# Performance work log

Hardware: AMD Instinct MI355X
Metric: run time of the kernel (lower is better)

The kernel has to match this reference:

```python
import jax, jax.numpy as jnp
import numpy as np
from jax.ops import segment_sum

N_NODES = 50000
N_EDGES = 400000
D_IN = 128
HIDDEN = [128, 128]
D_OUT = 64
ALPHA = 0.5


def _glorot(key, shape):
    fan_in, fan_out = shape
    lim = jnp.sqrt(6.0 / (fan_in + fan_out))
    return jax.random.uniform(key, shape, jnp.float32, -lim, lim)


def setup_inputs() -> dict:
    key = jax.random.key(0)
    ks = jax.random.split(key, 16)
    x = jax.random.normal(ks[0], (N_NODES, D_IN), jnp.float32)
    edge_index = jax.random.randint(ks[1], (2, N_EDGES), 0, N_NODES, jnp.int64)
    theta = jax.random.uniform(ks[2], (N_EDGES,), jnp.float32)
    return {
        "x": x,
        "edge_index": edge_index,
        "theta": theta,
        "W1_s2d": _glorot(ks[3], (D_IN, HIDDEN[0])),
        "W1_d2s": _glorot(ks[4], (D_IN, HIDDEN[0])),
        "b1_s2d": jnp.zeros((HIDDEN[0],), jnp.float32),
        "b1_d2s": jnp.zeros((HIDDEN[0],), jnp.float32),
        "W2_s2d": _glorot(ks[5], (HIDDEN[0], HIDDEN[1])),
        "W2_d2s": _glorot(ks[6], (HIDDEN[0], HIDDEN[1])),
        "b2_s2d": jnp.zeros((HIDDEN[1],), jnp.float32),
        "b2_d2s": jnp.zeros((HIDDEN[1],), jnp.float32),
        "W_ro": _glorot(ks[7], (HIDDEN[1], D_OUT)),
        "b_ro": jnp.zeros((D_OUT,), jnp.float32),
    }


def _fuzzy_laplacian(edge_index, theta, num_nodes):
    # bidirectional duplication + self loops (self_loop=True, edge_weight=1)
    senders, receivers = edge_index[0], edge_index[1]
    loop = jnp.arange(num_nodes, dtype=senders.dtype)
    cs = jnp.concatenate((senders, receivers, loop))
    cr = jnp.concatenate((receivers, senders, loop))
    c2, s2 = jnp.cos(theta) ** 2, jnp.sin(theta) ** 2
    ones = jnp.ones((num_nodes,), theta.dtype)
    # real(e^{i t})^2 = cos^2 t ; exp(i(pi/2 - t)) -> real^2 = sin^2 t
    out_w = jnp.concatenate((c2, s2, ones))
    in_w = jnp.concatenate((s2, c2, ones))
    deg_s = segment_sum(out_w, cs, num_segments=num_nodes) + 1e-12
    deg_r = segment_sum(in_w, cs, num_segments=num_nodes) + 1e-12
    dis_s = jnp.where(deg_s > 1e11, 0.0, jax.lax.rsqrt(deg_s))
    dis_r = jnp.where(deg_r > 1e11, 0.0, jax.lax.rsqrt(deg_r))
    w_s2d = dis_s[cs] * out_w * dis_r[cr]
    w_d2s = dis_r[cs] * in_w * dis_s[cr]
    return cs, cr, w_s2d, w_d2s


def _forward(x, edge_index, theta, W1_s2d, W1_d2s, b1_s2d, b1_d2s,
             W2_s2d, W2_d2s, b2_s2d, b2_d2s, W_ro, b_ro):
    num_nodes = x.shape[0]
    cs, cr, w_s2d, w_d2s = _fuzzy_laplacian(edge_index, theta, num_nodes)
    layers = [(W1_s2d, W1_d2s, b1_s2d, b1_d2s), (W2_s2d, W2_d2s, b2_s2d, b2_d2s)]
    for Ws, Wd, bs, bd in layers:
        xs = x[cs]  # [2E+N, F] gather
        agg_s = segment_sum(xs * w_s2d[:, None], cr, num_segments=num_nodes)
        agg_d = segment_sum(xs * w_d2s[:, None], cr, num_segments=num_nodes)
        x = ALPHA * (agg_s @ Ws + bs) + (1.0 - ALPHA) * (agg_d @ Wd + bd)
        x = jax.nn.relu(x)
    return x @ W_ro + b_ro


def reference(x, edge_index, theta, W1_s2d, W1_d2s, b1_s2d, b1_d2s,
              W2_s2d, W2_d2s, b2_s2d, b2_d2s, W_ro, b_ro):
    return _forward(x, edge_index, theta, W1_s2d, W1_d2s, b1_s2d, b1_d2s,
                    W2_s2d, W2_d2s, b2_s2d, b2_d2s, W_ro, b_ro)
```

## Files before the change

### kernel.cpp

```cpp
#include <hip/hip_runtime.h>
#include <hip/hip_fp16.h>

#define N_NODES 50000
#define N_EDGES 400000
#define CSR_E (2 * N_EDGES + N_NODES)
#define NCH 10
#define CHW 5000
#define NE2 (N_NODES * NCH)
#define EB 1563
#define PB 288

typedef unsigned short ushort_t;
typedef unsigned int uint_t;
typedef __attribute__((ext_vector_type(8))) short bf16x8;
typedef __attribute__((ext_vector_type(4))) float f32x4;

__device__ __forceinline__ float bf2f(ushort_t u) {
    return __uint_as_float(((uint_t)u) << 16);
}
__device__ __forceinline__ ushort_t f2bf(float f) {
    uint_t b = __float_as_uint(f);
    b += 0x7FFFu + ((b >> 16) & 1u);
    return (ushort_t)(b >> 16);
}
__device__ __forceinline__ uint_t packw(float a, float b) {
    return ((uint_t)__half_as_ushort(__float2half(b)) << 16) |
           (uint_t)__half_as_ushort(__float2half(a));
}
__device__ __forceinline__ float unpl(uint_t w) {
    return __half2float(__ushort_as_half((ushort_t)(w & 0xffffu)));
}
__device__ __forceinline__ float unph(uint_t w) {
    return __half2float(__ushort_as_half((ushort_t)(w >> 16)));
}


__device__ int g_est;
__device__ int g_is16;
__device__ __align__(8) float2 g_dis2[N_NODES];
__device__ int g_cnt2[NE2];
__device__ int g_offs2[NE2 + 1];
__device__ uint_t g_rank[N_EDGES];
__device__ uint_t g_scanst[512];
__device__ __align__(16) uint4 g_estage[N_EDGES];
__device__ __align__(16) uint2 g_csr8[CSR_E];
__device__ __align__(16) ushort_t g_h1[(size_t)N_NODES * 128];
__device__ __align__(16) ushort_t g_xcvt[(size_t)N_NODES * 128];
__device__ __align__(16) ushort_t g_bp1[8 * 128 * 32];
__device__ __align__(16) ushort_t g_bp2[8 * 128 * 32];
__device__ __align__(16) ushort_t g_bp3[4 * 64 * 32];
__device__ float g_bc1[128];
__device__ float g_bc2[128];
__device__ float g_bro[64];


__global__ __launch_bounds__(256) void init_all(const uint_t* __restrict__ xw,
                                                const int* __restrict__ eidx,
                                                const float* __restrict__ x32) {
    __shared__ int s_flags;
    if (threadIdx.x < 64) {
        uint_t w = xw[threadIdx.x];
        int elo = (w >> 7) & 0xFF;
        unsigned long long mb = __ballot(elo >= 100 && elo <= 150);
        unsigned long long me = __ballot(eidx[2 * threadIdx.x + 1] != 0);
        if (threadIdx.x == 0) {
            int is16 = (__popcll(mb) >= 48) ? 1 : 0;
            int est = me ? 1 : 2;
            s_flags = is16 | (est << 1);
        }
    }
    __syncthreads();
    int is16 = s_flags & 1;
    int t = blockIdx.x * 256 + threadIdx.x;
    if (t == 0) {
        g_is16 = is16;
        g_est = s_flags >> 1;
    }
    if (t < 512) g_scanst[t] = 0;
    if (t < N_NODES) {
        int sc = t / CHW;
#pragma unroll
        for (int c = 0; c < NCH; c++) g_cnt2[t * NCH + c] = (c == sc) ? 1 : 0;
    }
    if (!is16 && t < N_NODES * 128 / 8) {
        const float4* p = (const float4*)(x32 + t * 8);
        float4 a = p[0], b = p[1];
        ushort4 o0, o1;
        o0.x = f2bf(a.x); o0.y = f2bf(a.y); o0.z = f2bf(a.z); o0.w = f2bf(a.w);
        o1.x = f2bf(b.x); o1.y = f2bf(b.y); o1.z = f2bf(b.z); o1.w = f2bf(b.w);
        *(ushort4*)(g_xcvt + t * 8) = o0;
        *(ushort4*)(g_xcvt + t * 8 + 4) = o1;
    }
}


__global__ __launch_bounds__(256) void edge_prep(
    const int* __restrict__ eidx, const ushort_t* __restrict__ th16, const float* __restrict__ th32,
    const ushort_t* W1s16, const float* W1s32, const ushort_t* W1d16, const float* W1d32,
    const ushort_t* b1s16, const float* b1s32, const ushort_t* b1d16, const float* b1d32,
    const ushort_t* W2s16, const float* W2s32, const ushort_t* W2d16, const float* W2d32,
    const ushort_t* b2s16, const float* b2s32, const ushort_t* b2d16, const float* b2d32,
    const ushort_t* Wro16, const float* Wro32, const ushort_t* bro16, const float* bro32) {
    int gb = blockIdx.x;
    if (gb < EB) {
        int e = gb * 256 + threadIdx.x;
        if (e >= N_EDGES) return;
        int st = g_est;
        int s = eidx[(size_t)e * st];
        int r = eidx[((size_t)N_EDGES + e) * st];
        float t = g_is16 ? bf2f(th16[e]) : th32[e];
        float sn, cs_;
        sincosf(t, &sn, &cs_);
        float c2 = cs_ * cs_;
        float s2 = sn * sn;
        g_estage[e] = make_uint4((uint_t)s, (uint_t)r, __float_as_uint(c2), __float_as_uint(s2));
        int rf = atomicAdd(&g_cnt2[r * NCH + s / CHW], 1);
        int rr = atomicAdd(&g_cnt2[s * NCH + r / CHW], 1);
        g_rank[e] = (uint_t)rf | ((uint_t)rr << 16);
        return;
    }
    int is16 = g_is16;
    int t = (gb - EB) * 256 + threadIdx.x;
    if (t < 2 * 32768) {
        int layer = t >> 15;
        int i = t & 32767;
        const ushort_t* Ws16 = layer ? W2s16 : W1s16;
        const float* Ws32 = layer ? W2s32 : W1s32;
        const ushort_t* Wd16 = layer ? W2d16 : W1d16;
        const float* Wd32 = layer ? W2d32 : W1d32;
        ushort_t* Bp = layer ? g_bp2 : g_bp1;
        int k = i >> 7, n = i & 127;
        ushort_t v;
        if (k < 128) {
            int idx = k * 128 + n;
            v = is16 ? Ws16[idx] : f2bf(Ws32[idx]);
        } else {
            int idx = (k - 128) * 128 + n;
            v = is16 ? Wd16[idx] : f2bf(Wd32[idx]);
        }
        int kb = k >> 5, kk = k & 31;
        Bp[((kb * 128 + n) << 5) + kk] = v;
        if (i < 128) {
            const ushort_t* bs16 = layer ? b2s16 : b1s16;
            const float* bs32 = layer ? b2s32 : b1s32;
            const ushort_t* bd16 = layer ? b2d16 : b1d16;
            const float* bd32 = layer ? b2d32 : b1d32;
            float a = is16 ? bf2f(bs16[i]) : bs32[i];
            float b = is16 ? bf2f(bd16[i]) : bd32[i];
            (layer ? g_bc2 : g_bc1)[i] = 0.5f * (a + b);
        }
    } else {
        int i = t - 2 * 32768;
        int k = i >> 6, n = i & 63;
        ushort_t v = is16 ? Wro16[i] : f2bf(Wro32[i]);
        int kb = k >> 5, kk = k & 31;
        g_bp3[((kb * 64 + n) << 5) + kk] = v;
        if (i < 64) g_bro[i] = is16 ? bf2f(bro16[i]) : bro32[i];
    }
}


__global__ __launch_bounds__(1024) void scan_lb() {
    __shared__ int sd[1024];
    __shared__ int s_ex;
    int b = blockIdx.x;
    int t = threadIdx.x;
    int i = b * 1024 + t;
    int v = (i < NE2) ? g_cnt2[i] : 0;
    sd[t] = v;
    __syncthreads();
    for (int o = 1; o < 1024; o <<= 1) {
        int tv = (t >= o) ? sd[t - o] : 0;
        __syncthreads();
        sd[t] += tv;
        __syncthreads();
    }
    int incl = sd[t];
    int agg = sd[1023];
    if (t == 0) {
        atomicExch(&g_scanst[b], ((b == 0 ? 2u : 1u) << 20) | (uint_t)agg);
    }
    if (t < 64) {
        int ex = 0;
        if (b > 0) {
            int j = b - 1;
            while (true) {
                int idx = j - 63 + t;
                uint_t wv = (idx >= 0) ? atomicAdd(&g_scanst[idx], 0u) : (2u << 20);
                uint_t fl = wv >> 20;
                unsigned long long m2 = __ballot(fl == 2u);
                unsigned long long m0 = __ballot(fl == 0u);
                if (m2 != 0ull) {
                    int p = 63 - __clzll(m2);
                    unsigned long long above = (p == 63) ? 0ull : (~0ull << (p + 1));
                    if ((m0 & above) != 0ull) continue;
                    int contrib = (t >= p) ? (int)(wv & 0xFFFFFu) : 0;
#pragma unroll
                    for (int o = 1; o < 64; o <<= 1) contrib += __shfl_xor(contrib, o);
                    ex += contrib;
                    break;
                } else {
                    if (m0 != 0ull) continue;
                    int contrib = (int)(wv & 0xFFFFFu);
#pragma unroll
                    for (int o = 1; o < 64; o <<= 1) contrib += __shfl_xor(contrib, o);
                    ex += contrib;
                    j -= 64;
                }
            }
        }
        if (t == 0) {
            atomicExch(&g_scanst[b], (2u << 20) | (uint_t)(ex + agg));
            s_ex = ex;
        }
    }
    __syncthreads();
    if (i < NE2) g_offs2[i] = incl - v + s_ex;
    if (b == 0 && t == 0) g_offs2[NE2] = CSR_E;
}


__global__ __launch_bounds__(256) void fill_all() {
    int e = blockIdx.x * 256 + threadIdx.x;
    if (e < N_EDGES) {
        uint4 stg = g_estage[e];
        int s = (int)stg.x;
        int r = (int)stg.y;
        float c2 = __uint_as_float(stg.z);
        float s2 = __uint_as_float(stg.w);
        uint_t rk = g_rank[e];
        int pf = g_offs2[r * NCH + s / CHW] + (int)(rk & 0xffffu);
        int pr = g_offs2[s * NCH + r / CHW] + (int)(rk >> 16);
        g_csr8[pf] = make_uint2((uint_t)s, packw(c2, s2));
        g_csr8[pr] = make_uint2((uint_t)r, packw(s2, c2));
    }
    if (e < N_NODES) {
        g_csr8[g_offs2[e * NCH + e / CHW]] = make_uint2((uint_t)e, packw(1.0f, 1.0f));
    }
}


__global__ __launch_bounds__(256) void deg_pass() {
    int n = blockIdx.x * 256 + threadIdx.x;
    if (n >= N_NODES) return;
    int kb = g_offs2[n * NCH];
    int ke = g_offs2[n * NCH + NCH];
    float ds = 0.f, dr = 0.f;
    for (int k = kb; k < ke; k++) {
        uint_t w = g_csr8[k].y;
        ds += unph(w);
        dr += unpl(w);
    }
    g_dis2[n] = make_float2(rsqrtf(ds + 1e-12f), rsqrtf(dr + 1e-12f));
}


template <int LAYER>
__global__ __launch_bounds__(256) void fused_layer(const ushort_t* __restrict__ xext,
                                                   void* __restrict__ outp) {
    __shared__ ushort_t tA[16 * 256];
    __shared__ ushort_t tH[(LAYER == 1) ? 16 * 128 : 1];
    int w = threadIdx.x >> 6;
    int lane = threadIdx.x & 63;
    int gsel = lane >> 4;
    int r = lane & 15;
    int lrow = w * 4 + gsel;
    int node = blockIdx.x * 16 + lrow;
    const ushort_t* xin = (LAYER == 0) ? (g_is16 ? xext : g_xcvt) : g_h1;

    int ks = g_offs2[node * NCH];
    int ke = g_offs2[node * NCH + NCH];
    int c0 = ke - ks;
    int cmax = c0;
    cmax = max(cmax, __shfl_xor(cmax, 16));
    cmax = max(cmax, __shfl_xor(cmax, 32));

    float accS[8], accD[8];
#pragma unroll
    for (int f = 0; f < 8; f++) { accS[f] = 0.f; accD[f] = 0.f; }

    uint2 ecur = g_csr8[ks + min(r, c0 - 1)];
    int lbase = lane & 48;
    for (int k = 0; k < cmax; k += 16) {
        uint2 enext = ecur;
        if (k + 16 < cmax) enext = g_csr8[ks + min(k + 16 + r, c0 - 1)];
#pragma unroll
        for (int h = 0; h < 4; h++) {
            int kh = k + h * 4;
            if (kh >= cmax) break;
            uint_t eys[4];
            float2 ds2[4];
            bf16x8 vs[4];
#pragma unroll
            for (int j = 0; j < 4; j++) {
                int jj = h * 4 + j;
                uint_t ex = (uint_t)__shfl((int)ecur.x, lbase | jj, 64);
                eys[j] = (uint_t)__shfl((int)ecur.y, lbase | jj, 64);
                ds2[j] = g_dis2[ex];
                vs[j] = *(const bf16x8*)(xin + (size_t)ex * 128 + r * 8);
            }
#pragma unroll
            for (int j = 0; j < 4; j++) {
                bool val = (kh + j) < c0;
                float ws_ = val ? ds2[j].x * unpl(eys[j]) : 0.f;
                float wd_ = val ? ds2[j].y * unph(eys[j]) : 0.f;
#pragma unroll
                for (int f = 0; f < 8; f++) {
                    float xv = bf2f((ushort_t)vs[j][f]);
                    accS[f] = fmaf(ws_, xv, accS[f]);
                    accD[f] = fmaf(wd_, xv, accD[f]);
                }
            }
        }
        ecur = enext;
    }

    float2 dn = g_dis2[node];
    float fs = 0.5f * dn.y;
    float fd = 0.5f * dn.x;
    uint_t oS[4], oD[4];
#pragma unroll
    for (int p = 0; p < 4; p++) {
        oS[p] = ((uint_t)f2bf(accS[2 * p + 1] * fs) << 16) | (uint_t)f2bf(accS[2 * p] * fs);
        oD[p] = ((uint_t)f2bf(accD[2 * p + 1] * fd) << 16) | (uint_t)f2bf(accD[2 * p] * fd);
    }
    int swA = (lrow & 7) << 4;
    *(uint4*)((char*)tA + ((lrow * 512 + r * 16) ^ swA)) = make_uint4(oS[0], oS[1], oS[2], oS[3]);
    *(uint4*)((char*)tA + ((lrow * 512 + 256 + r * 16) ^ swA)) = make_uint4(oD[0], oD[1], oD[2], oD[3]);
    __syncthreads();

    int cc = lane & 15;
    int q = lane >> 4;
    int csw = (cc & 7) << 4;
    const ushort_t* Bp = (LAYER == 0) ? g_bp1 : g_bp2;
    const float* bias = (LAYER == 0) ? g_bc1 : g_bc2;
    f32x4 acc0 = {0.f, 0.f, 0.f, 0.f};
    f32x4 acc1 = {0.f, 0.f, 0.f, 0.f};
#pragma unroll
    for (int kb = 0; kb < 8; kb++) {
        bf16x8 a = *(const bf16x8*)((const char*)tA + ((cc * 512 + kb * 64 + q * 16) ^ csw));
        bf16x8 b0 = *(const bf16x8*)(Bp + (((kb * 128 + w * 32 + cc) << 5) + q * 8));
        bf16x8 b1 = *(const bf16x8*)(Bp + (((kb * 128 + w * 32 + 16 + cc) << 5) + q * 8));
        acc0 = __builtin_amdgcn_mfma_f32_16x16x32_bf16(a, b0, acc0, 0, 0, 0);
        acc1 = __builtin_amdgcn_mfma_f32_16x16x32_bf16(a, b1, acc1, 0, 0, 0);
    }
    int mb = blockIdx.x * 16;
    float bi0 = bias[w * 32 + cc];
    float bi1 = bias[w * 32 + 16 + cc];
    if (LAYER == 0) {
#pragma unroll
        for (int rr = 0; rr < 4; rr++) {
            int m = mb + q * 4 + rr;
            g_h1[(size_t)m * 128 + w * 32 + cc] = f2bf(fmaxf(acc0[rr] + bi0, 0.f));
            g_h1[(size_t)m * 128 + w * 32 + 16 + cc] = f2bf(fmaxf(acc1[rr] + bi1, 0.f));
        }
    } else {
#pragma unroll
        for (int rr = 0; rr < 4; rr++) {
            int ml = q * 4 + rr;
            int msw = (ml & 7) << 4;
            *(ushort_t*)((char*)tH + ((ml * 256 + (w * 32 + cc) * 2) ^ msw)) =
                f2bf(fmaxf(acc0[rr] + bi0, 0.f));
            *(ushort_t*)((char*)tH + ((ml * 256 + (w * 32 + 16 + cc) * 2) ^ msw)) =
                f2bf(fmaxf(acc1[rr] + bi1, 0.f));
        }
        __syncthreads();
        f32x4 a3 = {0.f, 0.f, 0.f, 0.f};
#pragma unroll
        for (int kb = 0; kb < 4; kb++) {
            bf16x8 a = *(const bf16x8*)((const char*)tH + ((cc * 256 + kb * 64 + q * 16) ^ csw));
            bf16x8 b = *(const bf16x8*)(g_bp3 + (((kb * 64 + w * 16 + cc) << 5) + q * 8));
            a3 = __builtin_amdgcn_mfma_f32_16x16x32_bf16(a, b, a3, 0, 0, 0);
        }
        int is16 = g_is16;
        float bi = g_bro[w * 16 + cc];
#pragma unroll
        for (int rr = 0; rr < 4; rr++) {
            int m = mb + q * 4 + rr;
            float v = a3[rr] + bi;
            if (is16)
                ((ushort_t*)outp)[(size_t)m * 64 + w * 16 + cc] = f2bf(v);
            else
                ((float*)outp)[(size_t)m * 64 + w * 16 + cc] = v;
        }
    }
}


static inline int cdiv(int a, int b) { return (a + b - 1) / b; }

extern "C" void kernel_launch(void* const* d_in, const int* in_sizes, int n_in,
                              void* d_out, int out_size, void* d_ws, size_t ws_size,
                              hipStream_t stream) {
    const void* x = d_in[0];
    const int* eidx = (const int*)d_in[1];
    const void* theta = d_in[2];
    const void* W1s = d_in[3];
    const void* W1d = d_in[4];
    const void* b1s = d_in[5];
    const void* b1d = d_in[6];
    const void* W2s = d_in[7];
    const void* W2d = d_in[8];
    const void* b2s = d_in[9];
    const void* b2d = d_in[10];
    const void* Wro = d_in[11];
    const void* bro = d_in[12];
    (void)in_sizes; (void)n_in; (void)out_size; (void)d_ws; (void)ws_size;

    const int NB2 = cdiv(NE2, 1024);

    init_all<<<cdiv(N_NODES * 128 / 8, 256), 256, 0, stream>>>(
        (const uint_t*)x, eidx, (const float*)x);
    edge_prep<<<EB + PB, 256, 0, stream>>>(
        eidx, (const ushort_t*)theta, (const float*)theta,
        (const ushort_t*)W1s, (const float*)W1s, (const ushort_t*)W1d, (const float*)W1d,
        (const ushort_t*)b1s, (const float*)b1s, (const ushort_t*)b1d, (const float*)b1d,
        (const ushort_t*)W2s, (const float*)W2s, (const ushort_t*)W2d, (const float*)W2d,
        (const ushort_t*)b2s, (const float*)b2s, (const ushort_t*)b2d, (const float*)b2d,
        (const ushort_t*)Wro, (const float*)Wro, (const ushort_t*)bro, (const float*)bro);
    scan_lb<<<NB2, 1024, 0, stream>>>();
    fill_all<<<cdiv(N_EDGES, 256), 256, 0, stream>>>();
    deg_pass<<<cdiv(N_NODES, 256), 256, 0, stream>>>();

    const int AB = N_NODES / 16;
    fused_layer<0><<<AB, 256, 0, stream>>>((const ushort_t*)x, nullptr);
    fused_layer<1><<<AB, 256, 0, stream>>>(nullptr, d_out);
}
```

Measured before the change: 263.1 us.

## Fold init into edge_prep, pre-scale CSR weights, pack rank into staging

Merges the init kernel into edge_prep. The x fp32-to-bf16 conversion runs as extra grid-strided blocks, and the count/scan-state reset moves into scan_lb and fill_all so state is reset for the next call. It drops the separate rank buffer by storing it in the staging record's fourth word and recomputes sin² as 1-cos². A new finalize_w pass multiplies the source-node normalisation into the packed fp16 edge weights, so both fused layers no longer gather g_dis2 per edge. The cost is one extra pass over the CSR array, plus fp16 rounding of the pre-multiplied weights.

Measured after the change: 260.0 us. No clear change (-1.2%).

```diff
diff --git a/kernel.cpp b/kernel.cpp
--- a/kernel.cpp
+++ b/kernel.cpp
@@ -9,6 +9,7 @@
 #define NE2 (N_NODES * NCH)
 #define EB 1563
 #define PB 288
+#define CB 1024
 
 typedef unsigned short ushort_t;
 typedef unsigned int uint_t;
@@ -40,7 +41,6 @@
 __device__ __align__(8) float2 g_dis2[N_NODES];
 __device__ int g_cnt2[NE2];
 __device__ int g_offs2[NE2 + 1];
-__device__ uint_t g_rank[N_EDGES];
 __device__ uint_t g_scanst[512];
 __device__ __align__(16) uint4 g_estage[N_EDGES];
 __device__ __align__(16) uint2 g_csr8[CSR_E];
@@ -54,9 +54,14 @@
 __device__ float g_bro[64];
 
 
-__global__ __launch_bounds__(256) void init_all(const uint_t* __restrict__ xw,
-                                                const int* __restrict__ eidx,
-                                                const float* __restrict__ x32) {
+__global__ __launch_bounds__(256) void edge_prep(
+    const uint_t* __restrict__ xw,
+    const int* __restrict__ eidx, const ushort_t* __restrict__ th16, const float* __restrict__ th32,
+    const ushort_t* W1s16, const float* W1s32, const ushort_t* W1d16, const float* W1d32,
+    const ushort_t* b1s16, const float* b1s32, const ushort_t* b1d16, const float* b1d32,
+    const ushort_t* W2s16, const float* W2s32, const ushort_t* W2d16, const float* W2d32,
+    const ushort_t* b2s16, const float* b2s32, const ushort_t* b2d16, const float* b2d32,
+    const ushort_t* Wro16, const float* Wro32, const ushort_t* bro16, const float* bro32) {
     __shared__ int s_flags;
     if (threadIdx.x < 64) {
         uint_t w = xw[threadIdx.x];
@@ -64,98 +69,85 @@
         unsigned long long mb = __ballot(elo >= 100 && elo <= 150);
         unsigned long long me = __ballot(eidx[2 * threadIdx.x + 1] != 0);
         if (threadIdx.x == 0) {
-            int is16 = (__popcll(mb) >= 48) ? 1 : 0;
-            int est = me ? 1 : 2;
-            s_flags = is16 | (est << 1);
+            int is16v = (__popcll(mb) >= 48) ? 1 : 0;
+            int estv = me ? 1 : 2;
+            s_flags = is16v | (estv << 1);
         }
     }
     __syncthreads();
     int is16 = s_flags & 1;
-    int t = blockIdx.x * 256 + threadIdx.x;
-    if (t == 0) {
+    int est = s_flags >> 1;
+    int gb = blockIdx.x;
+    if (gb == 0 && threadIdx.x == 0) {
         g_is16 = is16;
-        g_est = s_flags >> 1;
-    }
-    if (t < 512) g_scanst[t] = 0;
-    if (t < N_NODES) {
-        int sc = t / CHW;
-#pragma unroll
-        for (int c = 0; c < NCH; c++) g_cnt2[t * NCH + c] = (c == sc) ? 1 : 0;
-    }
-    if (!is16 && t < N_NODES * 128 / 8) {
-        const float4* p = (const float4*)(x32 + t * 8);
+        g_est = est;
+    }
+    if (gb < EB) {
+        int e = gb * 256 + threadIdx.x;
+        if (e >= N_EDGES) return;
+        int s = eidx[(size_t)e * est];
+        int r = eidx[((size_t)N_EDGES + e) * est];
+        float t = is16 ? bf2f(th16[e]) : th32[e];
+        float sn, cs_;
+        sincosf(t, &sn, &cs_);
+        float c2 = cs_ * cs_;
+        int rf = atomicAdd(&g_cnt2[r * NCH + s / CHW], 1);
+        int rr = atomicAdd(&g_cnt2[s * NCH + r / CHW], 1);
+        g_estage[e] = make_uint4((uint_t)s, (uint_t)r, __float_as_uint(c2),
+                                 (uint_t)rf | ((uint_t)rr << 16));
+        return;
+    }
+    if (gb < EB + PB) {
+        int t = (gb - EB) * 256 + threadIdx.x;
+        if (t < 2 * 32768) {
+            int layer = t >> 15;
+            int i = t & 32767;
+            const ushort_t* Ws16 = layer ? W2s16 : W1s16;
+            const float* Ws32 = layer ? W2s32 : W1s32;
+            const ushort_t* Wd16 = layer ? W2d16 : W1d16;
+            const float* Wd32 = layer ? W2d32 : W1d32;
+            ushort_t* Bp = layer ? g_bp2 : g_bp1;
+            int k = i >> 7, n = i & 127;
+            ushort_t v;
+            if (k < 128) {
+                int idx = k * 128 + n;
+                v = is16 ? Ws16[idx] : f2bf(Ws32[idx]);
+            } else {
+                int idx = (k - 128) * 128 + n;
+                v = is16 ? Wd16[idx] : f2bf(Wd32[idx]);
+            }
+            int kb = k >> 5, kk = k & 31;
+            Bp[((kb * 128 + n) << 5) + kk] = v;
+            if (i < 128) {
+                const ushort_t* bs16 = layer ? b2s16 : b1s16;
+                const float* bs32 = layer ? b2s32 : b1s32;
+                const ushort_t* bd16 = layer ? b2d16 : b1d16;
+                const float* bd32 = layer ? b2d32 : b1d32;
+                float a = is16 ? bf2f(bs16[i]) : bs32[i];
+                float b = is16 ? bf2f(bd16[i]) : bd32[i];
+                (layer ? g_bc2 : g_bc1)[i] = 0.5f * (a + b);
+            }
+        } else {
+            int i = t - 2 * 32768;
+            int k = i >> 6, n = i & 63;
+            ushort_t v = is16 ? Wro16[i] : f2bf(Wro32[i]);
+            int kb = k >> 5, kk = k & 31;
+            g_bp3[((kb * 64 + n) << 5) + kk] = v;
+            if (i < 64) g_bro[i] = is16 ? bf2f(bro16[i]) : bro32[i];
+        }
+        return;
+    }
+    if (is16) return;
+    const float* x32 = (const float*)xw;
+    const int total = N_NODES * 128 / 8;
+    for (int i = (gb - EB - PB) * 256 + threadIdx.x; i < total; i += CB * 256) {
+        const float4* p = (const float4*)(x32 + (size_t)i * 8);
         float4 a = p[0], b = p[1];
         ushort4 o0, o1;
         o0.x = f2bf(a.x); o0.y = f2bf(a.y); o0.z = f2bf(a.z); o0.w = f2bf(a.w);
         o1.x = f2bf(b.x); o1.y = f2bf(b.y); o1.z = f2bf(b.z); o1.w = f2bf(b.w);
-        *(ushort4*)(g_xcvt + t * 8) = o0;
-        *(ushort4*)(g_xcvt + t * 8 + 4) = o1;
-    }
-}
-
-
-__global__ __launch_bounds__(256) void edge_prep(
-    const int* __restrict__ eidx, const ushort_t* __restrict__ th16, const float* __restrict__ th32,
-    const ushort_t* W1s16, const float* W1s32, const ushort_t* W1d16, const float* W1d32,
-    const ushort_t* b1s16, const float* b1s32, const ushort_t* b1d16, const float* b1d32,
-    const ushort_t* W2s16, const float* W2s32, const ushort_t* W2d16, const float* W2d32,
-    const ushort_t* b2s16, const float* b2s32, const ushort_t* b2d16, const float* b2d32,
-    const ushort_t* Wro16, const float* Wro32, const ushort_t* bro16, const float* bro32) {
-    int gb = blockIdx.x;
-    if (gb < EB) {
-        int e = gb * 256 + threadIdx.x;
-        if (e >= N_EDGES) return;
-        int st = g_est;
-        int s = eidx[(size_t)e * st];
-        int r = eidx[((size_t)N_EDGES + e) * st];
-        float t = g_is16 ? bf2f(th16[e]) : th32[e];
-        float sn, cs_;
-        sincosf(t, &sn, &cs_);
-        float c2 = cs_ * cs_;
-        float s2 = sn * sn;
-        g_estage[e] = make_uint4((uint_t)s, (uint_t)r, __float_as_uint(c2), __float_as_uint(s2));
-        int rf = atomicAdd(&g_cnt2[r * NCH + s / CHW], 1);
-        int rr = atomicAdd(&g_cnt2[s * NCH + r / CHW], 1);
-        g_rank[e] = (uint_t)rf | ((uint_t)rr << 16);
-        return;
-    }
-    int is16 = g_is16;
-    int t = (gb - EB) * 256 + threadIdx.x;
-    if (t < 2 * 32768) {
-        int layer = t >> 15;
-        int i = t & 32767;
-        const ushort_t* Ws16 = layer ? W2s16 : W1s16;
-        const float* Ws32 = layer ? W2s32 : W1s32;
-        const ushort_t* Wd16 = layer ? W2d16 : W1d16;
-        const float* Wd32 = layer ? W2d32 : W1d32;
-        ushort_t* Bp = layer ? g_bp2 : g_bp1;
-        int k = i >> 7, n = i & 127;
-        ushort_t v;
-        if (k < 128) {
-            int idx = k * 128 + n;
-            v = is16 ? Ws16[idx] : f2bf(Ws32[idx]);
-        } else {
-            int idx = (k - 128) * 128 + n;
-            v = is16 ? Wd16[idx] : f2bf(Wd32[idx]);
-        }
-        int kb = k >> 5, kk = k & 31;
-        Bp[((kb * 128 + n) << 5) + kk] = v;
-        if (i < 128) {
-            const ushort_t* bs16 = layer ? b2s16 : b1s16;
-            const float* bs32 = layer ? b2s32 : b1s32;
-            const ushort_t* bd16 = layer ? b2d16 : b1d16;
-            const float* bd32 = layer ? b2d32 : b1d32;
-            float a = is16 ? bf2f(bs16[i]) : bs32[i];
-            float b = is16 ? bf2f(bd16[i]) : bd32[i];
-            (layer ? g_bc2 : g_bc1)[i] = 0.5f * (a + b);
-        }
-    } else {
-        int i = t - 2 * 32768;
-        int k = i >> 6, n = i & 63;
-        ushort_t v = is16 ? Wro16[i] : f2bf(Wro32[i]);
-        int kb = k >> 5, kk = k & 31;
-        g_bp3[((kb * 64 + n) << 5) + kk] = v;
-        if (i < 64) g_bro[i] = is16 ? bf2f(bro16[i]) : bro32[i];
+        *(ushort4*)(g_xcvt + (size_t)i * 8) = o0;
+        *(ushort4*)(g_xcvt + (size_t)i * 8 + 4) = o1;
     }
 }
 
@@ -166,7 +158,13 @@
     int b = blockIdx.x;
     int t = threadIdx.x;
     int i = b * 1024 + t;
-    int v = (i < NE2) ? g_cnt2[i] : 0;
+    int v = 0;
+    if (i < NE2) {
+        int n = i / NCH;
+        int c = i - n * NCH;
+        v = g_cnt2[i] + ((c == n / CHW) ? 1 : 0);
+        g_cnt2[i] = 0;
+    }
     sd[t] = v;
     __syncthreads();
     for (int o = 1; o < 1024; o <<= 1) {
@@ -221,21 +219,23 @@
 
 
 __global__ __launch_bounds__(256) void fill_all() {
+    if (blockIdx.x == 0 && threadIdx.x < 512) g_scanst[threadIdx.x] = 0;
     int e = blockIdx.x * 256 + threadIdx.x;
     if (e < N_EDGES) {
         uint4 stg = g_estage[e];
         int s = (int)stg.x;
         int r = (int)stg.y;
         float c2 = __uint_as_float(stg.z);
-        float s2 = __uint_as_float(stg.w);
-        uint_t rk = g_rank[e];
+        float s2 = 1.0f - c2;
+        uint_t rk = stg.w;
         int pf = g_offs2[r * NCH + s / CHW] + (int)(rk & 0xffffu);
         int pr = g_offs2[s * NCH + r / CHW] + (int)(rk >> 16);
         g_csr8[pf] = make_uint2((uint_t)s, packw(c2, s2));
         g_csr8[pr] = make_uint2((uint_t)r, packw(s2, c2));
     }
     if (e < N_NODES) {
-        g_csr8[g_offs2[e * NCH + e / CHW]] = make_uint2((uint_t)e, packw(1.0f, 1.0f));
+        int b = e * NCH + e / CHW;
+        g_csr8[g_offs2[b + 1] - 1] = make_uint2((uint_t)e, packw(1.0f, 1.0f));
     }
 }
 
@@ -252,6 +252,15 @@
         dr += unpl(w);
     }
     g_dis2[n] = make_float2(rsqrtf(ds + 1e-12f), rsqrtf(dr + 1e-12f));
+}
+
+
+__global__ __launch_bounds__(256) void finalize_w() {
+    int i = blockIdx.x * 256 + threadIdx.x;
+    if (i >= CSR_E) return;
+    uint2 e = g_csr8[i];
+    float2 d = g_dis2[e.x];
+    ((uint_t*)g_csr8)[2 * (size_t)i + 1] = packw(d.x * unpl(e.y), d.y * unph(e.y));
 }
 
 
@@ -289,21 +298,19 @@
             int kh = k + h * 4;
             if (kh >= cmax) break;
             uint_t eys[4];
-            float2 ds2[4];
             bf16x8 vs[4];
 #pragma unroll
             for (int j = 0; j < 4; j++) {
                 int jj = h * 4 + j;
                 uint_t ex = (uint_t)__shfl((int)ecur.x, lbase | jj, 64);
                 eys[j] = (uint_t)__shfl((int)ecur.y, lbase | jj, 64);
-                ds2[j] = g_dis2[ex];
                 vs[j] = *(const bf16x8*)(xin + (size_t)ex * 128 + r * 8);
             }
 #pragma unroll
             for (int j = 0; j < 4; j++) {
                 bool val = (kh + j) < c0;
-                float ws_ = val ? ds2[j].x * unpl(eys[j]) : 0.f;
-                float wd_ = val ? ds2[j].y * unph(eys[j]) : 0.f;
+                float ws_ = val ? unpl(eys[j]) : 0.f;
+                float wd_ = val ? unph(eys[j]) : 0.f;
 #pragma unroll
                 for (int f = 0; f < 8; f++) {
                     float xv = bf2f((ushort_t)vs[j][f]);
@@ -409,10 +416,8 @@
 
     const int NB2 = cdiv(NE2, 1024);
 
-    init_all<<<cdiv(N_NODES * 128 / 8, 256), 256, 0, stream>>>(
-        (const uint_t*)x, eidx, (const float*)x);
-    edge_prep<<<EB + PB, 256, 0, stream>>>(
-        eidx, (const ushort_t*)theta, (const float*)theta,
+    edge_prep<<<EB + PB + CB, 256, 0, stream>>>(
+        (const uint_t*)x, eidx, (const ushort_t*)theta, (const float*)theta,
         (const ushort_t*)W1s, (const float*)W1s, (const ushort_t*)W1d, (const float*)W1d,
         (const ushort_t*)b1s, (const float*)b1s, (const ushort_t*)b1d, (const float*)b1d,
         (const ushort_t*)W2s, (const float*)W2s, (const ushort_t*)W2d, (const float*)W2d,
@@ -421,6 +426,7 @@
     scan_lb<<<NB2, 1024, 0, stream>>>();
     fill_all<<<cdiv(N_EDGES, 256), 256, 0, stream>>>();
     deg_pass<<<cdiv(N_NODES, 256), 256, 0, stream>>>();
+    finalize_w<<<cdiv(CSR_E, 256), 256, 0, stream>>>();
 
     const int AB = N_NODES / 16;
     fused_layer<0><<<AB, 256, 0, stream>>>((const ushort_t*)x, nullptr);
```
